# Performance work log

Measured on AMD Instinct MI355X. Metric: run time of the kernel, lower is better.

Reference implementation:

```python
import jax, jax.numpy as jnp
import numpy as np

T, B, IN, H, OUT = 512, 128, 64, 1024, 64


def _gru_layer(x, w_ih, w_hh, b_ih, b_hh):
    # x: (T, B, in_dim); w_ih: (3H, in_dim); w_hh: (3H, H); gate order: r, z, n (torch)
    gi = jnp.einsum('tbi,gi->tbg', x, w_ih) + b_ih  # (T, B, 3H) input-side gates, precomputed
    h0 = jnp.zeros((x.shape[1], w_hh.shape[1]), x.dtype)

    def step(h, gi_t):
        gh = h @ w_hh.T + b_hh                      # (B, 3H)
        ir, iz, inn = jnp.split(gi_t, 3, axis=-1)
        hr, hz, hn = jnp.split(gh, 3, axis=-1)
        r = jax.nn.sigmoid(ir + hr)
        z = jax.nn.sigmoid(iz + hz)
        n = jnp.tanh(inn + r * hn)
        h_new = (1.0 - z) * n + z * h
        return h_new, h_new

    _, out = jax.lax.scan(step, h0, gi)             # out: (T, B, H)
    return out


def setup_inputs() -> dict:
    key = jax.random.key(0)
    ks = jax.random.split(key, 11)
    s_in = 1.0 / np.sqrt(H)
    inp = {
        'x': jax.random.normal(ks[0], (T, B, IN), dtype=jnp.float32),
        'w_ih0': jax.random.uniform(ks[1], (3 * H, IN), jnp.float32, -s_in, s_in),
        'w_hh0': jax.random.uniform(ks[2], (3 * H, H), jnp.float32, -s_in, s_in),
        'b_ih0': jax.random.uniform(ks[3], (3 * H,), jnp.float32, -s_in, s_in),
        'b_hh0': jax.random.uniform(ks[4], (3 * H,), jnp.float32, -s_in, s_in),
        'w_ih1': jax.random.uniform(ks[5], (3 * H, H), jnp.float32, -s_in, s_in),
        'w_hh1': jax.random.uniform(ks[6], (3 * H, H), jnp.float32, -s_in, s_in),
        'b_ih1': jax.random.uniform(ks[7], (3 * H,), jnp.float32, -s_in, s_in),
        'b_hh1': jax.random.uniform(ks[8], (3 * H,), jnp.float32, -s_in, s_in),
        'w_lin': jax.random.uniform(ks[9], (OUT, H), jnp.float32, -s_in, s_in),
        'b_lin': jax.random.uniform(ks[10], (OUT,), jnp.float32, -s_in, s_in),
    }
    return inp


def reference(x, w_ih0, w_hh0, b_ih0, b_hh0, w_ih1, w_hh1, b_ih1, b_hh1, w_lin, b_lin):
    h1 = _gru_layer(x, w_ih0, w_hh0, b_ih0, b_hh0)   # (T, B, H)
    h2 = _gru_layer(h1, w_ih1, w_hh1, b_ih1, b_hh1)  # (T, B, H)
    out = jnp.einsum('tbh,oh->tbo', h2, w_lin) + b_lin  # time-distributed linear
    return out
```

## Files before the change

kernel.cpp:

```cpp
#include <hip/hip_runtime.h>

#define Tn  512
#define Bn  128
#define INn 64
#define Hn  1024

typedef __attribute__((ext_vector_type(8))) _Float16 f16x8;
typedef __attribute__((ext_vector_type(4))) float f32x4;
typedef unsigned short u16;

#define AGENT __HIP_MEMORY_SCOPE_AGENT

__device__ __forceinline__ u16 f2h(float f) {
  union { _Float16 h; u16 u; } v;
  v.h = (_Float16)f;
  return v.u;
}
__device__ __forceinline__ float sigmoidf_(float x) {
  return 1.0f / (1.0f + __expf(-x));
}
__device__ __forceinline__ float tanhf_(float x) {
  float e = __expf(-2.0f * fabsf(x));
  float t = (1.0f - e) / (1.0f + e);
  return copysignf(t, x);
}
__device__ __forceinline__ f32x4 mfma16(f16x8 a, f16x8 b, f32x4 c) {
  return __builtin_amdgcn_mfma_f32_16x16x32_f16(a, b, c, 0, 0, 0);
}
__device__ __forceinline__ size_t hidx(int row, int col) {
  return ((size_t)((row >> 4) * 32 + (col >> 5))) * 512 +
         ((((col >> 3) & 3) * 16 + (row & 15)) * 8) + (col & 7);
}
__device__ __forceinline__ void acq_fence() {
  __builtin_amdgcn_fence(__ATOMIC_ACQUIRE, "agent");
}
__device__ __forceinline__ void coh_store(u16* p, u16 a, u16 b) {
  __hip_atomic_store((unsigned*)p, (unsigned)a | ((unsigned)b << 16),
                     __ATOMIC_RELAXED, AGENT);
}
__device__ __forceinline__ void ldb4(f16x8 dst[4], const u16* __restrict__ h,
                                     size_t ab, int kc0) {
#pragma unroll
  for (int k = 0; k < 4; ++k)
    dst[k] = *(const f16x8*)(h + ab + (size_t)(kc0 + k) * 512);
}
__device__ __forceinline__ void fma12(f32x4 acc[3], const f16x8 b[4],
                                      const f16x8 W[3][8], int kc0) {
#pragma unroll
  for (int k = 0; k < 4; ++k) {
#pragma unroll
    for (int g = 0; g < 3; ++g)
      acc[g] = mfma16(b[k], W[g][kc0 + k], acc[g]);
  }
}

__global__ void pack_w(const float* __restrict__ s, u16* __restrict__ d, int R, int K) {
  int tid = blockIdx.x * blockDim.x + threadIdx.x;
  int total = (R * K) >> 3;
  if (tid >= total) return;
  int l = tid & 63;
  int ckc = tid >> 6;
  int nkc = K >> 5;
  int ct = ckc / nkc;
  int kc = ckc - ct * nkc;
  int row = ct * 16 + (l & 15);
  int k0 = kc * 32 + (l >> 4) * 8;
  const float* sp = s + (size_t)row * K + k0;
  float4 a = *(const float4*)sp;
  float4 b = *(const float4*)(sp + 4);
  f16x8 o;
  u16* op = (u16*)&o;
  op[0] = f2h(a.x); op[1] = f2h(a.y); op[2] = f2h(a.z); op[3] = f2h(a.w);
  op[4] = f2h(b.x); op[5] = f2h(b.y); op[6] = f2h(b.z); op[7] = f2h(b.w);
  *(f16x8*)(d + (size_t)tid * 8) = o;
}

__global__ void zero16(uint4* __restrict__ p, int n4) {
  int i = blockIdx.x * blockDim.x + threadIdx.x;
  if (i < n4) p[i] = make_uint4(0u, 0u, 0u, 0u);
}

#define PS 131072

__global__ __launch_bounds__(512, 1) void gru_main(
    const float* __restrict__ x,
    const float* __restrict__ b_ih0, const float* __restrict__ b_hh0,
    const float* __restrict__ b_ih1, const float* __restrict__ b_hh1,
    const float* __restrict__ b_lin,
    const u16* __restrict__ wih0p, const u16* __restrict__ whh0p,
    const u16* __restrict__ wih1p, const u16* __restrict__ whh1p,
    const u16* __restrict__ wlinp,
    u16* __restrict__ hA, u16* __restrict__ hB,
    float* __restrict__ out, int* __restrict__ flags) {
  extern __shared__ float lds[];

  const int blk  = blockIdx.x;
  const int tid  = threadIdx.x;
  const int w    = tid >> 6;
  const int lane = tid & 63;
  const int ln   = lane & 15;
  const int lq   = lane >> 4;
  const int layer = blk >> 7;
  const int lb   = blk & 127;
  const f32x4 vz = {0.f, 0.f, 0.f, 0.f};

  if (layer == 0) {
    const int bg  = lb >> 5;
    const int hsl = lb & 31;
    const int q   = w & 1;
    const int kg  = w >> 1;
    const int c16 = hsl * 2 + q;
    const bool kgl = (kg < 2);
    const int xm  = kg;
    f16x8 W[3][8];
#pragma unroll
    for (int g = 0; g < 3; ++g)
#pragma unroll
      for (int kc = 0; kc < 8; ++kc)
        W[g][kc] = *(const f16x8*)(whh0p + (((size_t)(g * 64 + c16) * 32 + kg * 8 + kc) * 64 + lane) * 8);
    f16x8 Wx[3][2];
    if (kgl) {
#pragma unroll
      for (int g = 0; g < 3; ++g)
#pragma unroll
        for (int kc = 0; kc < 2; ++kc)
          Wx[g][kc] = *(const f16x8*)(wih0p + (((size_t)(g * 64 + c16) * 2 + kc) * 64 + lane) * 8);
    }
    const bool is_lin = (hsl < 8);
    const int lcg = hsl & 3;
    const int lrt = hsl >> 2;
    float Blin = 0.f;
    f16x8 Wl[4];
    if (is_lin) {
      Blin = b_lin[lcg * 16 + (tid & 15)];
#pragma unroll
      for (int kc = 0; kc < 4; ++kc)
        Wl[kc] = *(const f16x8*)(wlinp + (((size_t)lcg * 32 + w * 4 + kc) * 64 + lane) * 8);
    }
    const int rm  = tid >> 8;
    const int rr  = (tid >> 4) & 15;
    const int rc2 = (tid & 15) * 2;
    const int ggr = bg * 32 + rm * 16 + rr;
    float Br[2], Bz[2], Bni[2], Bnh[2];
#pragma unroll
    for (int e = 0; e < 2; ++e) {
      const int gc = hsl * 32 + rc2 + e;
      Br[e]  = b_ih0[gc] + b_hh0[gc];
      Bz[e]  = b_ih0[Hn + gc] + b_hh0[Hn + gc];
      Bni[e] = b_ih0[2 * Hn + gc];
      Bnh[e] = b_hh0[2 * Hn + gc];
    }
    const int* pPeer = flags + ((bg << 5) + (lane & 31)) * 32;
    const int* pBp   = flags + 4096 + (((bg >> 1) << 6) + lane) * 32;
    const size_t abL = ((size_t)(bg * 2 + lrt) * 32 + w * 4) * 512 + lane * 8;
    float h0prev[2] = {0.f, 0.f};

    for (int t = 0; t <= Tn + 7; ++t) {
      f16x8 lbuf[4];
      if (t < Tn) {
        if (w == 0) {
          for (;;) {
            bool ok = true;
            if (t > 0 && __hip_atomic_load(pPeer, __ATOMIC_RELAXED, AGENT) < t) ok = false;
            if (t >= 8 && __hip_atomic_load(pBp, __ATOMIC_RELAXED, AGENT) < t - 7) ok = false;
            if (!__all(ok)) { __builtin_amdgcn_s_sleep(1); continue; }
            break;
          }
          acq_fence();
        }
        __syncthreads();
        const int rs = (t + 7) & 7;
        const int ws_ = t & 7;
        const u16* Ahb = hA + (size_t)rs * PS;
        float4 xv0, xv1, xv2, xv3;
        if (kgl) {
          const float* xr = x + ((size_t)t * Bn + bg * 32 + xm * 16 + ln) * INn + lq * 8;
          xv0 = *(const float4*)xr;        xv1 = *(const float4*)(xr + 4);
          xv2 = *(const float4*)(xr + 32); xv3 = *(const float4*)(xr + 36);
        }
        f32x4 acc0[3] = {vz, vz, vz}, acc1[3] = {vz, vz, vz};
        f16x8 b0[4], b1[4], b2[4], b3[4];
        const size_t ab0 = ((size_t)(bg * 2 + 0) * 32 + kg * 8) * 512 + lane * 8;
        const size_t ab1 = ((size_t)(bg * 2 + 1) * 32 + kg * 8) * 512 + lane * 8;
        ldb4(b0, Ahb, ab0, 0);
        ldb4(b1, Ahb, ab0, 4);
        ldb4(b2, Ahb, ab1, 0);
        ldb4(b3, Ahb, ab1, 4);
        if (is_lin && t >= 8)
          ldb4(lbuf, hB + (size_t)((t - 8) & 7) * PS, abL, 0);
        fma12(acc0, b0, W, 0);
        fma12(acc0, b1, W, 4);
        fma12(acc1, b2, W, 0);
        fma12(acc1, b3, W, 4);
        {
          float* Hp0 = lds + (size_t)(0 * 4 + kg) * 1680;
          float* Hp1 = lds + (size_t)(1 * 4 + kg) * 1680;
#pragma unroll
          for (int g = 0; g < 3; ++g)
#pragma unroll
            for (int i = 0; i < 4; ++i) {
              Hp0[g * 560 + (lq * 4 + i) * 35 + q * 16 + ln] = acc0[g][i];
              Hp1[g * 560 + (lq * 4 + i) * 35 + q * 16 + ln] = acc1[g][i];
            }
        }
        if (kgl) {
          f16x8 a0, a1;
          u16* a0p = (u16*)&a0;
          u16* a1p = (u16*)&a1;
          a0p[0] = f2h(xv0.x); a0p[1] = f2h(xv0.y); a0p[2] = f2h(xv0.z); a0p[3] = f2h(xv0.w);
          a0p[4] = f2h(xv1.x); a0p[5] = f2h(xv1.y); a0p[6] = f2h(xv1.z); a0p[7] = f2h(xv1.w);
          a1p[0] = f2h(xv2.x); a1p[1] = f2h(xv2.y); a1p[2] = f2h(xv2.z); a1p[3] = f2h(xv2.w);
          a1p[4] = f2h(xv3.x); a1p[5] = f2h(xv3.y); a1p[6] = f2h(xv3.z); a1p[7] = f2h(xv3.w);
          f32x4 ax[3] = {vz, vz, vz};
#pragma unroll
          for (int g = 0; g < 3; ++g) {
            ax[g] = mfma16(a0, Wx[g][0], ax[g]);
            ax[g] = mfma16(a1, Wx[g][1], ax[g]);
          }
          float* Ip = lds + 13440 + (size_t)xm * 1680;
#pragma unroll
          for (int g = 0; g < 3; ++g)
#pragma unroll
            for (int i = 0; i < 4; ++i)
              Ip[g * 560 + (lq * 4 + i) * 35 + q * 16 + ln] = ax[g][i];
        }
        __syncthreads();
        {
          u16* whp = hA + (size_t)ws_ * PS;
          const size_t idx0 = hidx(ggr, hsl * 32 + rc2);
          u16 hh[2];
#pragma unroll
          for (int e = 0; e < 2; ++e) {
            const int c = rc2 + e;
            const float* Ip = lds + 13440 + (size_t)rm * 1680 + rr * 35 + c;
            float I0 = Ip[0], I1 = Ip[560], I2 = Ip[1120];
            float H0 = 0.f, H1 = 0.f, H2 = 0.f;
#pragma unroll
            for (int kgi = 0; kgi < 4; ++kgi) {
              const float* Hp = lds + (size_t)(rm * 4 + kgi) * 1680 + rr * 35 + c;
              H0 += Hp[0]; H1 += Hp[560]; H2 += Hp[1120];
            }
            float r  = sigmoidf_(I0 + H0 + Br[e]);
            float zz = sigmoidf_(I1 + H1 + Bz[e]);
            float nn = tanhf_(I2 + Bni[e] + r * (H2 + Bnh[e]));
            float hv = (1.0f - zz) * nn + zz * h0prev[e];
            h0prev[e] = hv;
            hh[e] = f2h(hv);
          }
          coh_store(whp + idx0, hh[0], hh[1]);
        }
        __syncthreads();
        if (tid == 0)
          __hip_atomic_store(flags + ((bg << 5) + hsl) * 32, t + 1, __ATOMIC_RELAXED, AGENT);
      } else if (is_lin) {
        if (w == 0) {
          while (!__all(__hip_atomic_load(pBp, __ATOMIC_RELAXED, AGENT) >= t - 7))
            __builtin_amdgcn_s_sleep(1);
          acq_fence();
        }
        __syncthreads();
        ldb4(lbuf, hB + (size_t)((t - 8) & 7) * PS, abL, 0);
      }
      if (is_lin && t >= 8) {
        const int s2 = t - 8;
        f32x4 la = vz;
#pragma unroll
        for (int k = 0; k < 4; ++k)
          la = mfma16(lbuf[k], Wl[k], la);
        __syncthreads();
        if (tid == 0)
          __hip_atomic_store(flags + 8192 + ((bg << 3) + hsl) * 32, s2 + 1, __ATOMIC_RELAXED, AGENT);
#pragma unroll
        for (int i = 0; i < 4; ++i)
          lds[(w * 16 + lq * 4 + i) * 21 + ln] = la[i];
        __syncthreads();
        if (tid < 256) {
          const int lr = (tid >> 4) & 15, lc = tid & 15;
          float s = Blin;
#pragma unroll
          for (int w8 = 0; w8 < 8; ++w8)
            s += lds[(w8 * 16 + lr) * 21 + lc];
          out[((size_t)s2 * Bn + bg * 32 + lrt * 16 + lr) * 64 + lcg * 16 + lc] = s;
        }
      }
    }
  } else {
    const int cs  = lb >> 1;
    const int rh  = lb & 1;
    const int side = w >> 2;
    const int ks  = w & 3;
    const u16* wsrc = side ? whh1p : wih1p;
    f16x8 W[3][8];
#pragma unroll
    for (int g = 0; g < 3; ++g)
#pragma unroll
      for (int kc = 0; kc < 8; ++kc)
        W[g][kc] = *(const f16x8*)(wsrc + (((size_t)(g * 64 + cs) * 32 + ks * 8 + kc) * 64 + lane) * 8);
    const int mq  = tid >> 7;
    const int er  = (tid >> 3) & 15;
    const int ec0 = (tid & 7) * 2;
    float Br2[2], Bz2[2], Bni2[2], Bnh2[2];
#pragma unroll
    for (int e = 0; e < 2; ++e) {
      const int g2 = cs * 16 + ec0 + e;
      Br2[e]  = b_ih1[g2] + b_hh1[g2];
      Bz2[e]  = b_ih1[Hn + g2] + b_hh1[Hn + g2];
      Bni2[e] = b_ih1[2 * Hn + g2];
      Bnh2[e] = b_hh1[2 * Hn + g2];
    }
    const size_t idxE = hidx(rh * 64 + mq * 16 + er, cs * 16 + ec0);
    float h1prev[2] = {0.f, 0.f};
    const int* pA = flags + ((rh << 6) + lane) * 32;
    const int* pB = flags + 4096 + ((rh << 6) + lane) * 32;
    const int* pC = flags + 8192 + ((rh << 4) + (lane & 15)) * 32;

    for (int s = 0; s < Tn; ++s) {
      if (w == 0) {
        for (;;) {
          bool ok = __hip_atomic_load(pA, __ATOMIC_RELAXED, AGENT) >= s + 1;
          if (s >= 8 && (lane & 15) == lane &&
              __hip_atomic_load(pC, __ATOMIC_RELAXED, AGENT) < s - 7) ok = false;
          if (__all(ok)) break;
          __builtin_amdgcn_s_sleep(1);
        }
        acq_fence();
      }
      __syncthreads();
      const int ss = s & 7;
      const int rs = (s + 7) & 7;
      const u16* A1h = hA + (size_t)ss * PS;
      const u16* A2h = hB + (size_t)rs * PS;
      u16* whp = hB + (size_t)ss * PS;
      const u16* Ahb = side ? A2h : A1h;
      if (side && s > 0) {
        while (!__all(__hip_atomic_load(pB, __ATOMIC_RELAXED, AGENT) >= s))
          __builtin_amdgcn_s_sleep(1);
      }
      f32x4 acc0[3] = {vz, vz, vz}, acc1[3] = {vz, vz, vz};
      f32x4 acc2[3] = {vz, vz, vz}, acc3[3] = {vz, vz, vz};
      f16x8 b0[4], b1[4], b2[4], b3[4];
      const int mA = rh * 4;
      const size_t abT0 = ((size_t)(mA + 0) * 32 + ks * 8) * 512 + lane * 8;
      const size_t abT1 = ((size_t)(mA + 1) * 32 + ks * 8) * 512 + lane * 8;
      const size_t abT2 = ((size_t)(mA + 2) * 32 + ks * 8) * 512 + lane * 8;
      const size_t abT3 = ((size_t)(mA + 3) * 32 + ks * 8) * 512 + lane * 8;
      ldb4(b0, Ahb, abT0, 0);
      ldb4(b1, Ahb, abT0, 4);
      ldb4(b2, Ahb, abT1, 0);
      ldb4(b3, Ahb, abT1, 4);
      fma12(acc0, b0, W, 0);
      ldb4(b0, Ahb, abT2, 0);
      fma12(acc0, b1, W, 4);
      ldb4(b1, Ahb, abT2, 4);
      fma12(acc1, b2, W, 0);
      ldb4(b2, Ahb, abT3, 0);
      fma12(acc1, b3, W, 4);
      ldb4(b3, Ahb, abT3, 4);
      fma12(acc2, b0, W, 0);
      fma12(acc2, b1, W, 4);
      fma12(acc3, b2, W, 0);
      fma12(acc3, b3, W, 4);
#pragma unroll
      for (int g = 0; g < 3; ++g)
#pragma unroll
        for (int i = 0; i < 4; ++i) {
          const int ro = (lq * 4 + i) * 21 + ln;
          lds[((0 * 8 + w) * 3 + g) * 336 + ro] = acc0[g][i];
          lds[((1 * 8 + w) * 3 + g) * 336 + ro] = acc1[g][i];
          lds[((2 * 8 + w) * 3 + g) * 336 + ro] = acc2[g][i];
          lds[((3 * 8 + w) * 3 + g) * 336 + ro] = acc3[g][i];
        }
      __syncthreads();
      {
        u16 hh[2];
#pragma unroll
        for (int e = 0; e < 2; ++e) {
          const int rc = ec0 + e;
          float I0 = 0.f, I1 = 0.f, I2 = 0.f, H0 = 0.f, H1 = 0.f, H2 = 0.f;
#pragma unroll
          for (int wi = 0; wi < 4; ++wi) {
            const float* P = lds + ((mq * 8 + wi) * 3) * 336 + er * 21 + rc;
            I0 += P[0]; I1 += P[336]; I2 += P[672];
          }
#pragma unroll
          for (int wi = 4; wi < 8; ++wi) {
            const float* P = lds + ((mq * 8 + wi) * 3) * 336 + er * 21 + rc;
            H0 += P[0]; H1 += P[336]; H2 += P[672];
          }
          float r  = sigmoidf_(I0 + H0 + Br2[e]);
          float zz = sigmoidf_(I1 + H1 + Bz2[e]);
          float nn = tanhf_(I2 + Bni2[e] + r * (H2 + Bnh2[e]));
          float hv = (1.0f - zz) * nn + zz * h1prev[e];
          h1prev[e] = hv;
          hh[e] = f2h(hv);
        }
        coh_store(whp + idxE, hh[0], hh[1]);
      }
      __syncthreads();
      if (tid == 0)
        __hip_atomic_store(flags + 4096 + ((rh << 6) + cs) * 32, s + 1, __ATOMIC_RELAXED, AGENT);
    }
  }
}

extern "C" void kernel_launch(void* const* d_in, const int* in_sizes, int n_in,
                              void* d_out, int out_size, void* d_ws, size_t ws_size,
                              hipStream_t stream) {
  (void)in_sizes; (void)n_in; (void)out_size; (void)ws_size;
  const float* x     = (const float*)d_in[0];
  const float* wih0f = (const float*)d_in[1];
  const float* whh0f = (const float*)d_in[2];
  const float* bih0  = (const float*)d_in[3];
  const float* bhh0  = (const float*)d_in[4];
  const float* wih1f = (const float*)d_in[5];
  const float* whh1f = (const float*)d_in[6];
  const float* bih1  = (const float*)d_in[7];
  const float* bhh1  = (const float*)d_in[8];
  const float* wlinf = (const float*)d_in[9];
  const float* blin  = (const float*)d_in[10];
  float* out = (float*)d_out;

  char* w = (char*)d_ws;
  u16* whh0p = (u16*)w; w += (size_t)3072 * 1024 * 2;
  u16* wih1p = (u16*)w; w += (size_t)3072 * 1024 * 2;
  u16* whh1p = (u16*)w; w += (size_t)3072 * 1024 * 2;
  u16* wih0p = (u16*)w; w += (size_t)3072 * 64 * 2;
  u16* wlinp = (u16*)w; w += (size_t)64 * 1024 * 2;
  u16* hA    = (u16*)w; w += (size_t)8 * PS * 2;
  u16* hB    = (u16*)w; w += (size_t)8 * PS * 2;
  int* flags = (int*)w; w += 36864;

  static int attr_done = 0;
  if (!attr_done) {
    (void)hipFuncSetAttribute((const void*)gru_main,
                              hipFuncAttributeMaxDynamicSharedMemorySize, 131072);
    attr_done = 1;
  }

  const int thr = 256;
  pack_w<<<(3072 * 1024 / 8 + thr - 1) / thr, thr, 0, stream>>>(whh0f, whh0p, 3072, 1024);
  pack_w<<<(3072 * 1024 / 8 + thr - 1) / thr, thr, 0, stream>>>(wih1f, wih1p, 3072, 1024);
  pack_w<<<(3072 * 1024 / 8 + thr - 1) / thr, thr, 0, stream>>>(whh1f, whh1p, 3072, 1024);
  pack_w<<<(3072 * 64 / 8 + thr - 1) / thr, thr, 0, stream>>>(wih0f, wih0p, 3072, 64);
  pack_w<<<(64 * 1024 / 8 + thr - 1) / thr, thr, 0, stream>>>(wlinf, wlinp, 64, 1024);
  const int n4 = (int)(((size_t)16 * PS * 2 + 36864) / 16);
  zero16<<<(n4 + thr - 1) / thr, thr, 0, stream>>>((uint4*)hA, n4);

  void* args[] = {(void*)&x,     (void*)&bih0,  (void*)&bhh0,  (void*)&bih1,  (void*)&bhh1,
                  (void*)&blin,  (void*)&wih0p, (void*)&whh0p, (void*)&wih1p, (void*)&whh1p,
                  (void*)&wlinp, (void*)&hA,    (void*)&hB,    (void*)&out,   (void*)&flags};
  hipLaunchCooperativeKernel((const void*)gru_main, dim3(256), dim3(512), args, 129024, stream);
}
```

Before: 4.083 ms.

## Use write-once per-timestep hidden-state planes to drop ring backpressure waits

When the workspace is large enough, a templated kernel variant gives every timestep its own hidden-state plane instead of an 8-deep ring buffer. Slots are never reused, so the backpressure waits between layers and the linear stage (pBp/pC checks, linear-done flags) and the acquire fences are dropped. This removes cross-block stalls on the recurrent critical path. It costs a much larger workspace and more scattered memory traffic, and dropping the acquire fences relies on relaxed loads still seeing fresh data.

```diff
diff --git a/kernel.cpp b/kernel.cpp
--- a/kernel.cpp
+++ b/kernel.cpp
@@ -82,6 +82,7 @@
 
 #define PS 131072
 
+template <bool WO>
 __global__ __launch_bounds__(512, 1) void gru_main(
     const float* __restrict__ x,
     const float* __restrict__ b_ih0, const float* __restrict__ b_hh0,
@@ -159,19 +160,18 @@
       f16x8 lbuf[4];
       if (t < Tn) {
         if (w == 0) {
+          const bool needB = WO ? (is_lin && t >= 8) : (t >= 8);
           for (;;) {
             bool ok = true;
             if (t > 0 && __hip_atomic_load(pPeer, __ATOMIC_RELAXED, AGENT) < t) ok = false;
-            if (t >= 8 && __hip_atomic_load(pBp, __ATOMIC_RELAXED, AGENT) < t - 7) ok = false;
+            if (needB && __hip_atomic_load(pBp, __ATOMIC_RELAXED, AGENT) < t - 7) ok = false;
             if (!__all(ok)) { __builtin_amdgcn_s_sleep(1); continue; }
             break;
           }
-          acq_fence();
-        }
-        __syncthreads();
-        const int rs = (t + 7) & 7;
-        const int ws_ = t & 7;
-        const u16* Ahb = hA + (size_t)rs * PS;
+          if (!WO) acq_fence();
+        }
+        __syncthreads();
+        const u16* Ahb = hA + (size_t)(WO ? t : ((t + 7) & 7)) * PS;
         float4 xv0, xv1, xv2, xv3;
         if (kgl) {
           const float* xr = x + ((size_t)t * Bn + bg * 32 + xm * 16 + ln) * INn + lq * 8;
@@ -187,7 +187,7 @@
         ldb4(b2, Ahb, ab1, 0);
         ldb4(b3, Ahb, ab1, 4);
         if (is_lin && t >= 8)
-          ldb4(lbuf, hB + (size_t)((t - 8) & 7) * PS, abL, 0);
+          ldb4(lbuf, hB + (size_t)(WO ? (t - 7) : ((t - 8) & 7)) * PS, abL, 0);
         fma12(acc0, b0, W, 0);
         fma12(acc0, b1, W, 4);
         fma12(acc1, b2, W, 0);
@@ -226,7 +226,7 @@
         }
         __syncthreads();
         {
-          u16* whp = hA + (size_t)ws_ * PS;
+          u16* whp = hA + (size_t)(WO ? (t + 1) : (t & 7)) * PS;
           const size_t idx0 = hidx(ggr, hsl * 32 + rc2);
           u16 hh[2];
 #pragma unroll
@@ -256,10 +256,10 @@
         if (w == 0) {
           while (!__all(__hip_atomic_load(pBp, __ATOMIC_RELAXED, AGENT) >= t - 7))
             __builtin_amdgcn_s_sleep(1);
-          acq_fence();
-        }
-        __syncthreads();
-        ldb4(lbuf, hB + (size_t)((t - 8) & 7) * PS, abL, 0);
+          if (!WO) acq_fence();
+        }
+        __syncthreads();
+        ldb4(lbuf, hB + (size_t)(WO ? (t - 7) : ((t - 8) & 7)) * PS, abL, 0);
       }
       if (is_lin && t >= 8) {
         const int s2 = t - 8;
@@ -268,7 +268,7 @@
         for (int k = 0; k < 4; ++k)
           la = mfma16(lbuf[k], Wl[k], la);
         __syncthreads();
-        if (tid == 0)
+        if (!WO && tid == 0)
           __hip_atomic_store(flags + 8192 + ((bg << 3) + hsl) * 32, s2 + 1, __ATOMIC_RELAXED, AGENT);
 #pragma unroll
         for (int i = 0; i < 4; ++i)
@@ -318,19 +318,17 @@
       if (w == 0) {
         for (;;) {
           bool ok = __hip_atomic_load(pA, __ATOMIC_RELAXED, AGENT) >= s + 1;
-          if (s >= 8 && (lane & 15) == lane &&
+          if (!WO && s >= 8 && (lane & 15) == lane &&
               __hip_atomic_load(pC, __ATOMIC_RELAXED, AGENT) < s - 7) ok = false;
           if (__all(ok)) break;
           __builtin_amdgcn_s_sleep(1);
         }
-        acq_fence();
+        if (!WO) acq_fence();
       }
       __syncthreads();
-      const int ss = s & 7;
-      const int rs = (s + 7) & 7;
-      const u16* A1h = hA + (size_t)ss * PS;
-      const u16* A2h = hB + (size_t)rs * PS;
-      u16* whp = hB + (size_t)ss * PS;
+      const u16* A1h = hA + (size_t)(WO ? (s + 1) : (s & 7)) * PS;
+      const u16* A2h = hB + (size_t)(WO ? s : ((s + 7) & 7)) * PS;
+      u16* whp = hB + (size_t)(WO ? (s + 1) : (s & 7)) * PS;
       const u16* Ahb = side ? A2h : A1h;
       if (side && s > 0) {
         while (!__all(__hip_atomic_load(pB, __ATOMIC_RELAXED, AGENT) >= s))
@@ -406,7 +404,7 @@
 extern "C" void kernel_launch(void* const* d_in, const int* in_sizes, int n_in,
                               void* d_out, int out_size, void* d_ws, size_t ws_size,
                               hipStream_t stream) {
-  (void)in_sizes; (void)n_in; (void)out_size; (void)ws_size;
+  (void)in_sizes; (void)n_in; (void)out_size;
   const float* x     = (const float*)d_in[0];
   const float* wih0f = (const float*)d_in[1];
   const float* whh0f = (const float*)d_in[2];
@@ -420,21 +418,31 @@
   const float* blin  = (const float*)d_in[10];
   float* out = (float*)d_out;
 
+  const size_t wbytes = (size_t)3 * 3072 * 1024 * 2 + (size_t)3072 * 64 * 2 +
+                        (size_t)64 * 1024 * 2;
+  const size_t woNeed = wbytes + (size_t)2 * (Tn + 1) * PS * 2 + 36864;
+  bool wo = (ws_size >= woNeed);
+  const int planes = wo ? (Tn + 1) : 8;
+
   char* w = (char*)d_ws;
   u16* whh0p = (u16*)w; w += (size_t)3072 * 1024 * 2;
   u16* wih1p = (u16*)w; w += (size_t)3072 * 1024 * 2;
   u16* whh1p = (u16*)w; w += (size_t)3072 * 1024 * 2;
   u16* wih0p = (u16*)w; w += (size_t)3072 * 64 * 2;
   u16* wlinp = (u16*)w; w += (size_t)64 * 1024 * 2;
-  u16* hA    = (u16*)w; w += (size_t)8 * PS * 2;
-  u16* hB    = (u16*)w; w += (size_t)8 * PS * 2;
+  u16* hA    = (u16*)w; w += (size_t)planes * PS * 2;
+  u16* hB    = (u16*)w; w += (size_t)planes * PS * 2;
   int* flags = (int*)w; w += 36864;
 
-  static int attr_done = 0;
-  if (!attr_done) {
-    (void)hipFuncSetAttribute((const void*)gru_main,
+  if (wo) {
+    if (hipFuncSetAttribute((const void*)gru_main<true>,
+                            hipFuncAttributeMaxDynamicSharedMemorySize,
+                            131072) != hipSuccess)
+      wo = false;
+  }
+  if (!wo) {
+    (void)hipFuncSetAttribute((const void*)gru_main<false>,
                               hipFuncAttributeMaxDynamicSharedMemorySize, 131072);
-    attr_done = 1;
   }
 
   const int thr = 256;
@@ -443,11 +451,15 @@
   pack_w<<<(3072 * 1024 / 8 + thr - 1) / thr, thr, 0, stream>>>(whh1f, whh1p, 3072, 1024);
   pack_w<<<(3072 * 64 / 8 + thr - 1) / thr, thr, 0, stream>>>(wih0f, wih0p, 3072, 64);
   pack_w<<<(64 * 1024 / 8 + thr - 1) / thr, thr, 0, stream>>>(wlinf, wlinp, 64, 1024);
-  const int n4 = (int)(((size_t)16 * PS * 2 + 36864) / 16);
-  zero16<<<(n4 + thr - 1) / thr, thr, 0, stream>>>((uint4*)hA, n4);
+  const int zplanes = wo ? 1 : 8;
+  const int nzr = zplanes * PS * 2 / 16;
+  zero16<<<(nzr + thr - 1) / thr, thr, 0, stream>>>((uint4*)hA, nzr);
+  zero16<<<(nzr + thr - 1) / thr, thr, 0, stream>>>((uint4*)hB, nzr);
+  zero16<<<(36864 / 16 + thr - 1) / thr, thr, 0, stream>>>((uint4*)flags, 36864 / 16);
 
   void* args[] = {(void*)&x,     (void*)&bih0,  (void*)&bhh0,  (void*)&bih1,  (void*)&bhh1,
                   (void*)&blin,  (void*)&wih0p, (void*)&whh0p, (void*)&wih1p, (void*)&whh1p,
                   (void*)&wlinp, (void*)&hA,    (void*)&hB,    (void*)&out,   (void*)&flags};
-  hipLaunchCooperativeKernel((const void*)gru_main, dim3(256), dim3(512), args, 129024, stream);
-}
+  const void* kfn = wo ? (const void*)gru_main<true> : (const void*)gru_main<false>;
+  hipLaunchCooperativeKernel(kfn, dim3(256), dim3(512), args, 129024, stream);
+}
```

New measurement: 4.088 ms. Within noise of the previous version (+0.1%).
